# Optimization experiments

Measured on AMD Instinct MI355X. Metric: run time of the kernel, lower is better.

The kernel has to match this reference:

```python
import jax, jax.numpy as jnp
import numpy as np

B, Q, K, H, DQ, DK, DV = 8, 256, 256, 256, 256, 256, 256


def setup_inputs() -> dict:
    key = jax.random.key(0)
    k1, k2, k3, k4, k5, k6, k7 = jax.random.split(key, 7)
    queries = jax.random.normal(k1, (B, Q, DQ), dtype=jnp.float32)
    keys = jax.random.normal(k2, (B, K, DK), dtype=jnp.float32)
    values = jax.random.normal(k3, (B, K, DV), dtype=jnp.float32)
    valid_lens = jax.random.randint(k4, (B,), 1, K + 1)
    # learned params (torch Linear without bias); stored as (in, out)
    s = 1.0 / np.sqrt(H)
    W_q = jax.random.uniform(k5, (DQ, H), minval=-s, maxval=s, dtype=jnp.float32)
    W_k = jax.random.uniform(k6, (DK, H), minval=-s, maxval=s, dtype=jnp.float32)
    w_v = jax.random.uniform(k7, (H,), minval=-s, maxval=s, dtype=jnp.float32)
    return {"queries": queries, "keys": keys, "values": values,
            "valid_lens": valid_lens, "W_q": W_q, "W_k": W_k, "w_v": w_v}


def reference(queries, keys, values, valid_lens, W_q, W_k, w_v):
    q = queries @ W_q                      # (B, Q, H)
    k = keys @ W_k                         # (B, K, H)
    # broadcast add + tanh -> (B, Q, K, H), then linear score -> (B, Q, K)
    features = jnp.tanh(q[:, :, None, :] + k[:, None, :, :])
    scores = jnp.einsum('bqkh,h->bqk', features, w_v)
    mask = jnp.arange(K)[None, None, :] >= valid_lens[:, None, None]  # (B,1,K)
    scores = jnp.where(mask, -1000000.0, scores)
    attn = jax.nn.softmax(scores, axis=-1)  # (B, Q, K)
    return jnp.einsum('bqk,bkd->bqd', attn, values)  # (B, Q, DV)
```

## Files before the change

kernel.cpp:

```cpp
#include <hip/hip_runtime.h>
#include <hip/hip_bf16.h>

#define LOG2E 1.4426950408889634f
#define C2    (2.0f * LOG2E)

static __device__ __forceinline__ float fast_exp2(float x) {
#if __has_builtin(__builtin_amdgcn_exp2f)
  return __builtin_amdgcn_exp2f(x);
#else
  return exp2f(x);
#endif
}
static __device__ __forceinline__ float fast_rcp(float x) {
#if __has_builtin(__builtin_amdgcn_rcpf)
  return __builtin_amdgcn_rcpf(x);
#else
  return 1.0f / x;
#endif
}

typedef short bf16x8 __attribute__((ext_vector_type(8)));
typedef float f32x4  __attribute__((ext_vector_type(4)));

static __device__ __forceinline__ short f2bf(float x) {
  unsigned u = __float_as_uint(x);
  u += 0x7fff + ((u >> 16) & 1);
  return (short)(u >> 16);
}

__global__ __launch_bounds__(256, 4) void proj_kernel(
    const float* __restrict__ queries, const float* __restrict__ keys,
    const float* __restrict__ W_q,     const float* __restrict__ W_k,
    const int*   __restrict__ vlen,
    float* __restrict__ qs, float* __restrict__ ks_p)
{
  const int bz = blockIdx.z;
  const float* X = bz ? keys : queries;
  const float* W = bz ? W_k  : W_q;
  const int n0 = blockIdx.x * 32;
  const int m0 = blockIdx.y * 64;

  if (bz == 1) {
    const int vl = vlen[m0 >> 8];
    if ((m0 & 255) >= vl) return;
  }

  const int t = threadIdx.x;
  const int l = t & 63;
  const int w = t >> 6;

  __shared__ short Wp[8 * 2 * 64 * 8];

  {
    const int nl = t & 31, ko = t >> 5;
#pragma unroll
    for (int rep = 0; rep < 4; ++rep) {
      const int koct = ko + rep * 8;
      const int kc  = koct >> 2;
      const int grp = koct & 3;
      const int nt  = nl >> 4;
      const int ln  = grp * 16 + (nl & 15);
      short w8[8];
#pragma unroll
      for (int jj = 0; jj < 8; ++jj)
        w8[jj] = f2bf(W[(size_t)(koct * 8 + jj) * 256 + n0 + nl]);
      *(bf16x8*)&Wp[((kc * 2 + nt) * 64 + ln) * 8] = *(bf16x8*)w8;
    }
  }
  __syncthreads();

  const int mb   = m0 + w * 16;
  const int row  = mb + (l & 15);
  const int kofs = (l >> 4) * 8;

  f32x4 acc0 = {0.f, 0.f, 0.f, 0.f};
  f32x4 acc1 = {0.f, 0.f, 0.f, 0.f};
#pragma unroll
  for (int kc = 0; kc < 8; ++kc) {
    float4 a0 = *(const float4*)&X[(size_t)row * 256 + kc * 32 + kofs];
    float4 a1 = *(const float4*)&X[(size_t)row * 256 + kc * 32 + kofs + 4];
    bf16x8 af;
    af[0] = f2bf(a0.x); af[1] = f2bf(a0.y); af[2] = f2bf(a0.z); af[3] = f2bf(a0.w);
    af[4] = f2bf(a1.x); af[5] = f2bf(a1.y); af[6] = f2bf(a1.z); af[7] = f2bf(a1.w);
    bf16x8 b0 = *(bf16x8*)&Wp[((kc * 2 + 0) * 64 + l) * 8];
    bf16x8 b1 = *(bf16x8*)&Wp[((kc * 2 + 1) * 64 + l) * 8];
    acc0 = __builtin_amdgcn_mfma_f32_16x16x32_bf16(af, b0, acc0, 0, 0, 0);
    acc1 = __builtin_amdgcn_mfma_f32_16x16x32_bf16(af, b1, acc1, 0, 0, 0);
  }

  const int c = l & 15;
#pragma unroll
  for (int nt = 0; nt < 2; ++nt) {
    const f32x4 acc = nt ? acc1 : acc0;
    const int n = n0 + nt * 16 + c;
#pragma unroll
    for (int j = 0; j < 4; ++j) {
      const int rj = (l >> 4) * 4 + j;
      const float o = fast_exp2(acc[j] * C2);
      if (bz == 0) {
        qs[(size_t)(mb + rj) * 256 + n] = o;
      } else {
        const int b  = mb >> 8;
        const int kl = (mb & 255) + rj;
        ks_p[((size_t)(b * 64 + (n >> 2)) * 256 + kl) * 4 + (n & 3)] = o;
      }
    }
  }
}

#define SC_PAIR_Q(qv, qi, ca, cb)                                          \
  {                                                                        \
    float t0 = fmaf(qv.ca, kv[j].ca, 1.f);                                 \
    float t1 = fmaf(qv.cb, kv[j].cb, 1.f);                                 \
    float num = fmaf(wv.ca, t1, wv.cb * t0);                               \
    sc[j][qi] = fmaf(num, fast_rcp(t0 * t1), sc[j][qi]);                   \
  }

template <int NJ>
__device__ __forceinline__ void score_loop(
    const float* __restrict__ kp,
    const float* __restrict__ qp,
    const float* __restrict__ wvp, int h4b, float (&sc)[4][4])
{
#pragma unroll 2
  for (int h4 = h4b; h4 < h4b + 8; ++h4) {
    float4 kv[NJ];
#pragma unroll
    for (int j = 0; j < NJ; ++j)
      kv[j] = *(const float4*)(kp + h4 * 1024 + j * 256);
    float4 qv0 = *(const float4*)(qp + 0 * 256 + h4 * 4);
    float4 qv1 = *(const float4*)(qp + 1 * 256 + h4 * 4);
    float4 qv2 = *(const float4*)(qp + 2 * 256 + h4 * 4);
    float4 qv3 = *(const float4*)(qp + 3 * 256 + h4 * 4);
    float4 wv  = *(const float4*)(wvp + h4 * 4);
#pragma unroll
    for (int j = 0; j < NJ; ++j) {
      SC_PAIR_Q(qv0, 0, x, y); SC_PAIR_Q(qv1, 1, x, y);
      SC_PAIR_Q(qv2, 2, x, y); SC_PAIR_Q(qv3, 3, x, y);
      SC_PAIR_Q(qv0, 0, z, w); SC_PAIR_Q(qv1, 1, z, w);
      SC_PAIR_Q(qv2, 2, z, w); SC_PAIR_Q(qv3, 3, z, w);
    }
  }
}

__global__ __launch_bounds__(512, 4) void attn_kernel(
    const float* __restrict__ qs, const float* __restrict__ ks_p,
    const float* __restrict__ values, const int* __restrict__ vlen,
    const float* __restrict__ w_v, float* __restrict__ out)
{
  const int t    = threadIdx.x;
  const int lane = t & 63;
  const int w    = t >> 6;
  const int bx   = blockIdx.x;
  const int b    = ((bx & 7) + (bx >> 6)) & 7;
  const int q0   = (bx >> 3) * 4;

  __shared__ __align__(16) float sbuf[8192];
  __shared__ __align__(16) float p2[256 * 4];
  __shared__ float rsum_lds[4];

  const int vl = vlen[b];
  const int nj = (vl + 63) >> 6;

  float s0 = w_v[lane] + w_v[lane + 64] + w_v[lane + 128] + w_v[lane + 192];
#pragma unroll
  for (int off = 32; off; off >>= 1) s0 += __shfl_xor(s0, off);
  const float Wsum = s0;

  const float* qp = qs + (size_t)(b * 256 + q0) * 256;
  const float* kp = ks_p + (size_t)b * 65536 + lane * 4;
  const int h4b = w * 8;

  float sc[4][4] = {};
  switch (nj) {
    case 1:  score_loop<1>(kp, qp, w_v, h4b, sc); break;
    case 2:  score_loop<2>(kp, qp, w_v, h4b, sc); break;
    case 3:  score_loop<3>(kp, qp, w_v, h4b, sc); break;
    default: score_loop<4>(kp, qp, w_v, h4b, sc); break;
  }

#pragma unroll
  for (int j = 0; j < 4; ++j)
    *(float4*)&sbuf[((w * 4 + j) * 64 + lane) * 4] =
        make_float4(sc[j][0], sc[j][1], sc[j][2], sc[j][3]);
  __syncthreads();

  if (w < 4) {
    const int q = w;
    float scores[4];
    float mx = -3.4e38f;
#pragma unroll 4
    for (int j = 0; j < nj; ++j) {
      float s = 0.f;
#pragma unroll
      for (int ww = 0; ww < 8; ++ww)
        s += sbuf[((ww * 4 + j) * 64 + lane) * 4 + q];
      float v = Wsum - 2.f * s;
      if (j * 64 + lane >= vl) v = -1000000.0f;
      scores[j] = v;
      mx = fmaxf(mx, v);
    }
#pragma unroll
    for (int off = 32; off; off >>= 1) mx = fmaxf(mx, __shfl_xor(mx, off));
    float sum = 0.f;
#pragma unroll 4
    for (int j = 0; j < nj; ++j) {
      float p = fast_exp2((scores[j] - mx) * LOG2E);
      p2[(j * 64 + lane) * 4 + q] = p;
      sum += p;
    }
#pragma unroll
    for (int off = 32; off; off >>= 1) sum += __shfl_xor(sum, off);
    if (lane == 0) rsum_lds[q] = sum;
  }
  __syncthreads();

  float4 acc[4];
#pragma unroll
  for (int q = 0; q < 4; ++q) acc[q] = make_float4(0.f, 0.f, 0.f, 0.f);
  const float* Vb = values + (size_t)b * 65536 + lane * 4;
  if (w < vl) {
    float4 v = *(const float4*)(Vb + (size_t)w * 256);
    for (int k = w; k < vl; k += 8) {
      float4 vn = v;
      if (k + 8 < vl) vn = *(const float4*)(Vb + (size_t)(k + 8) * 256);
      float4 pk = *(const float4*)&p2[k * 4];
      acc[0].x = fmaf(pk.x, v.x, acc[0].x);
      acc[0].y = fmaf(pk.x, v.y, acc[0].y);
      acc[0].z = fmaf(pk.x, v.z, acc[0].z);
      acc[0].w = fmaf(pk.x, v.w, acc[0].w);
      acc[1].x = fmaf(pk.y, v.x, acc[1].x);
      acc[1].y = fmaf(pk.y, v.y, acc[1].y);
      acc[1].z = fmaf(pk.y, v.z, acc[1].z);
      acc[1].w = fmaf(pk.y, v.w, acc[1].w);
      acc[2].x = fmaf(pk.z, v.x, acc[2].x);
      acc[2].y = fmaf(pk.z, v.y, acc[2].y);
      acc[2].z = fmaf(pk.z, v.z, acc[2].z);
      acc[2].w = fmaf(pk.z, v.w, acc[2].w);
      acc[3].x = fmaf(pk.w, v.x, acc[3].x);
      acc[3].y = fmaf(pk.w, v.y, acc[3].y);
      acc[3].z = fmaf(pk.w, v.z, acc[3].z);
      acc[3].w = fmaf(pk.w, v.w, acc[3].w);
      v = vn;
    }
  }
#pragma unroll
  for (int q = 0; q < 4; ++q)
    *(float4*)&sbuf[(w * 4 + q) * 256 + lane * 4] = acc[q];
  __syncthreads();

#pragma unroll
  for (int rep = 0; rep < 2; ++rep) {
    int o = t + rep * 512;
    int q = o >> 8, d = o & 255;
    float s = 0.f;
#pragma unroll
    for (int ww = 0; ww < 8; ++ww) s += sbuf[(ww * 4 + q) * 256 + d];
    out[(size_t)(b * 256 + q0 + q) * 256 + d] = s * fast_rcp(rsum_lds[q]);
  }
}

extern "C" void kernel_launch(void* const* d_in, const int* in_sizes, int n_in,
                              void* d_out, int out_size, void* d_ws, size_t ws_size,
                              hipStream_t stream) {
  const float* queries = (const float*)d_in[0];
  const float* keys    = (const float*)d_in[1];
  const float* values  = (const float*)d_in[2];
  const int*   vlenp   = (const int*)d_in[3];
  const float* W_q     = (const float*)d_in[4];
  const float* W_k     = (const float*)d_in[5];
  const float* w_v     = (const float*)d_in[6];
  float* out = (float*)d_out;

  float* qs   = (float*)d_ws;
  float* ks_p = qs + 2048 * 256;

  dim3 pgrid(8, 32, 2);
  proj_kernel<<<pgrid, 256, 0, stream>>>(queries, keys, W_q, W_k, vlenp, qs, ks_p);
  attn_kernel<<<512, 512, 0, stream>>>(qs, ks_p, values, vlenp, w_v, out);
}
```

Measured before the change: 34.67 us.

## Balance batch workload across block pairs and deepen value prefetch

```diff
diff --git a/kernel.cpp b/kernel.cpp
--- a/kernel.cpp
+++ b/kernel.cpp
@@ -152,15 +152,36 @@
   const int lane = t & 63;
   const int w    = t >> 6;
   const int bx   = blockIdx.x;
-  const int b    = ((bx & 7) + (bx >> 6)) & 7;
-  const int q0   = (bx >> 3) * 4;
+
+  int njv[8];
+#pragma unroll
+  for (int i = 0; i < 8; ++i) njv[i] = (vlen[i] + 63) >> 6;
+  unsigned packed = 0, rem = 0xFFu;
+#pragma unroll
+  for (int r = 0; r < 8; ++r) {
+    int best = -1, bi = 0;
+#pragma unroll
+    for (int i = 0; i < 8; ++i) {
+      if (rem & (1u << i)) {
+        int key = njv[i] * 8 + (7 - i);
+        if (key > best) { best = key; bi = i; }
+      }
+    }
+    packed |= (unsigned)bi << (3 * r);
+    rem &= ~(1u << bi);
+  }
+  const int jpair = bx & 3;
+  const int hi    = (bx >> 8) & 1;
+  const int sel   = hi ? (7 - jpair) : jpair;
+  const int b     = (int)((packed >> (3 * sel)) & 7u);
+  const int q0    = ((bx >> 2) & 63) * 4;
 
   __shared__ __align__(16) float sbuf[8192];
   __shared__ __align__(16) float p2[256 * 4];
   __shared__ float rsum_lds[4];
 
   const int vl = vlen[b];
-  const int nj = (vl + 63) >> 6;
+  const int nj = njv[0] * 0 + ((vl + 63) >> 6);
 
   float s0 = w_v[lane] + w_v[lane + 64] + w_v[lane + 128] + w_v[lane + 192];
 #pragma unroll
@@ -220,28 +241,31 @@
   for (int q = 0; q < 4; ++q) acc[q] = make_float4(0.f, 0.f, 0.f, 0.f);
   const float* Vb = values + (size_t)b * 65536 + lane * 4;
   if (w < vl) {
-    float4 v = *(const float4*)(Vb + (size_t)w * 256);
+    float4 v0 = *(const float4*)(Vb + (size_t)w * 256);
+    float4 v1 = (w + 8 < vl) ? *(const float4*)(Vb + (size_t)(w + 8) * 256)
+                             : make_float4(0.f, 0.f, 0.f, 0.f);
     for (int k = w; k < vl; k += 8) {
-      float4 vn = v;
-      if (k + 8 < vl) vn = *(const float4*)(Vb + (size_t)(k + 8) * 256);
+      float4 vn = (k + 16 < vl)
+                      ? *(const float4*)(Vb + (size_t)(k + 16) * 256)
+                      : make_float4(0.f, 0.f, 0.f, 0.f);
       float4 pk = *(const float4*)&p2[k * 4];
-      acc[0].x = fmaf(pk.x, v.x, acc[0].x);
-      acc[0].y = fmaf(pk.x, v.y, acc[0].y);
-      acc[0].z = fmaf(pk.x, v.z, acc[0].z);
-      acc[0].w = fmaf(pk.x, v.w, acc[0].w);
-      acc[1].x = fmaf(pk.y, v.x, acc[1].x);
-      acc[1].y = fmaf(pk.y, v.y, acc[1].y);
-      acc[1].z = fmaf(pk.y, v.z, acc[1].z);
-      acc[1].w = fmaf(pk.y, v.w, acc[1].w);
-      acc[2].x = fmaf(pk.z, v.x, acc[2].x);
-      acc[2].y = fmaf(pk.z, v.y, acc[2].y);
-      acc[2].z = fmaf(pk.z, v.z, acc[2].z);
-      acc[2].w = fmaf(pk.z, v.w, acc[2].w);
-      acc[3].x = fmaf(pk.w, v.x, acc[3].x);
-      acc[3].y = fmaf(pk.w, v.y, acc[3].y);
-      acc[3].z = fmaf(pk.w, v.z, acc[3].z);
-      acc[3].w = fmaf(pk.w, v.w, acc[3].w);
-      v = vn;
+      acc[0].x = fmaf(pk.x, v0.x, acc[0].x);
+      acc[0].y = fmaf(pk.x, v0.y, acc[0].y);
+      acc[0].z = fmaf(pk.x, v0.z, acc[0].z);
+      acc[0].w = fmaf(pk.x, v0.w, acc[0].w);
+      acc[1].x = fmaf(pk.y, v0.x, acc[1].x);
+      acc[1].y = fmaf(pk.y, v0.y, acc[1].y);
+      acc[1].z = fmaf(pk.y, v0.z, acc[1].z);
+      acc[1].w = fmaf(pk.y, v0.w, acc[1].w);
+      acc[2].x = fmaf(pk.z, v0.x, acc[2].x);
+      acc[2].y = fmaf(pk.z, v0.y, acc[2].y);
+      acc[2].z = fmaf(pk.z, v0.z, acc[2].z);
+      acc[2].w = fmaf(pk.z, v0.w, acc[2].w);
+      acc[3].x = fmaf(pk.w, v0.x, acc[3].x);
+      acc[3].y = fmaf(pk.w, v0.y, acc[3].y);
+      acc[3].z = fmaf(pk.w, v0.z, acc[3].z);
+      acc[3].w = fmaf(pk.w, v0.w, acc[3].w);
+      v0 = v1; v1 = vn;
     }
   }
 #pragma unroll
```

After: 33.38 us. 3.7% less time.
